# Kernel tuning notes

Measured on AMD Instinct MI355X. Metric: run time of the kernel, lower is better.

## Reference

```python
import jax, jax.numpy as jnp
import numpy as np

B, C, N, T = 32, 32, 512, 168
EMB = 40
K_NEI = 20
ALPHA = 3.0          # saturation rate in graph learning
GCN_DEPTH = 2
PROP_ALPHA = 0.05    # retaining ratio in mix-hop propagation
KERNELS = (2, 3, 6, 7)
DIL = 2
T_OUT = T - (max(KERNELS) - 1) * DIL   # 156
C_BR = C // len(KERNELS)               # 8 channels per inception branch
EPS = 1e-5


def _conv2d(x, w, b, dil):
    # x: (B,Cin,N,T), w: (Cout,Cin,1,k), temporal dilation dil
    y = jax.lax.conv_general_dilated(
        x, w, window_strides=(1, 1), padding='VALID',
        rhs_dilation=(1, dil), dimension_numbers=('NCHW', 'OIHW', 'NCHW'))
    return y + b[None, :, None, None]


def _inception(x, ws, bs):
    outs = [_conv2d(x, w, b, DIL) for w, b in zip(ws, bs)]
    tmin = outs[-1].shape[-1]   # largest kernel -> shortest output
    return jnp.concatenate([o[..., -tmin:] for o in outs], axis=1)


def setup_inputs() -> dict:
    key = jax.random.key(0)
    ks = jax.random.split(key, 32)
    d = {}
    d['x'] = jax.random.normal(ks[0], (B, C, N, T), jnp.float32)
    d['idx'] = jnp.arange(N)  # permutation of nodes (identity)
    # graph learning params
    d['emb1'] = jax.random.normal(ks[1], (N, EMB), jnp.float32)
    d['emb2'] = jax.random.normal(ks[2], (N, EMB), jnp.float32)
    d['W1'] = jax.random.normal(ks[3], (EMB, EMB), jnp.float32) * 0.15
    d['b1'] = jnp.zeros((EMB,), jnp.float32)
    d['W2'] = jax.random.normal(ks[4], (EMB, EMB), jnp.float32) * 0.15
    d['b2'] = jnp.zeros((EMB,), jnp.float32)
    # dilated inception filter/gate conv params
    i = 5
    for pre in ('f', 'g'):
        for k in KERNELS:
            d[f'{pre}w{k}'] = jax.random.normal(ks[i], (C_BR, C, 1, k), jnp.float32) * 0.05
            d[f'{pre}b{k}'] = jnp.zeros((C_BR,), jnp.float32)
            i += 1
    # mix-hop 1x1 mlp: (gcn_depth+1)*C -> C
    d['mlp_w'] = jax.random.normal(ks[i], (C, (GCN_DEPTH + 1) * C, 1, 1), jnp.float32) * 0.05
    d['mlp_b'] = jnp.zeros((C,), jnp.float32)
    # node-indexed layer norm affine params, shape (C, N, T_OUT)
    d['ln_w'] = jnp.ones((C, N, T_OUT), jnp.float32)
    d['ln_b'] = jnp.zeros((C, N, T_OUT), jnp.float32)
    return d


def reference(x, idx, emb1, emb2, W1, b1, W2, b2,
              fw2, fb2, fw3, fb3, fw6, fb6, fw7, fb7,
              gw2, gb2, gw3, gb3, gw6, gb6, gw7, gb7,
              mlp_w, mlp_b, ln_w, ln_b):
    # ---- graph learning: topk-masked adjacency (N,N) ----
    n1 = jnp.tanh(ALPHA * (emb1[idx] @ W1.T + b1))
    n2 = jnp.tanh(ALPHA * (emb2[idx] @ W2.T + b2))
    a = n1 @ n2.T - n2 @ n1.T
    A = jax.nn.relu(jnp.tanh(ALPHA * a))
    _, top_idx = jax.lax.top_k(A, K_NEI)                 # deterministic topk (torch adds rand*0.01 tiebreak)
    mask = jnp.zeros_like(A).at[jnp.arange(A.shape[0])[:, None], top_idx].set(1.0)
    A = A * mask

    # ---- dilated inception gated temporal conv ----
    filt = jnp.tanh(_inception(x, (fw2, fw3, fw6, fw7), (fb2, fb3, fb6, fb7)))
    gate = jax.nn.sigmoid(_inception(x, (gw2, gw3, gw6, gw7), (gb2, gb3, gb6, gb7)))
    z = filt * gate                                       # (B, C, N, T_OUT)

    # ---- mix-hop graph convolution ----
    Ah = A + jnp.eye(A.shape[0], dtype=A.dtype)
    Ah = Ah / Ah.sum(1, keepdims=True)                    # row-degree normalization
    h = z
    hops = [z]
    for _ in range(GCN_DEPTH):
        h = PROP_ALPHA * z + (1.0 - PROP_ALPHA) * jnp.einsum('bcwt,vw->bcvt', h, Ah)
        hops.append(h)
    h0 = jnp.concatenate(hops, axis=1)                    # (B, 3C, N, T_OUT)
    out = _conv2d(h0, mlp_w, mlp_b, 1)                    # 1x1 mlp -> (B, C, N, T_OUT)

    # ---- residual + node-indexed layer norm over dims (C,N,T) ----
    out = out + x[..., -T_OUT:]
    mean = out.mean(axis=(1, 2, 3), keepdims=True)
    var = out.var(axis=(1, 2, 3), keepdims=True)
    out = (out - mean) * jax.lax.rsqrt(var + EPS)
    out = out * ln_w[:, idx, :][None] + ln_b[:, idx, :][None]
    return out
```

## Files before the change

### kernel.cpp

```cpp
#include <hip/hip_runtime.h>

#define NB 32
#define NC 32
#define NNODE 512
#define NT 168
#define NTO 156
#define NQ 39
#define NEMB 40
#define KNEI 20
#define NADJ 21
#define ZT_PITCH 42
#define XROWS 176
#define NPB 4
#define CT (NC * NTO)
#define NPAIR (CT / 8)

static_assert(NTO == 4 * NQ, "t quads");

typedef __attribute__((ext_vector_type(8))) short bf16x8;
typedef __attribute__((ext_vector_type(16))) float f32x16;
typedef __attribute__((ext_vector_type(4))) float f32x4;
typedef __attribute__((ext_vector_type(8))) unsigned short u16x8;

__device__ __forceinline__ float fast_tanh(float x) {
  float e = __expf(2.0f * x);
  return 1.0f - 2.0f / (e + 1.0f);
}
__device__ __forceinline__ float fast_sigmoid(float x) {
  return 1.0f / (1.0f + __expf(-x));
}
__device__ __forceinline__ unsigned short f2b(float v) {
  unsigned int u = __float_as_uint(v);
  unsigned int r = (u + 0x7FFFu + ((u >> 16) & 1u)) >> 16;
  return (unsigned short)r;
}
__device__ __forceinline__ float b2f(unsigned short u) {
  return __uint_as_float((unsigned int)u << 16);
}
template <typename T>
__device__ __forceinline__ void pin(T& v) {
  f32x4 t = __builtin_bit_cast(f32x4, v);
  asm volatile("" : "+v"(t));
  v = __builtin_bit_cast(T, t);
}

__global__ __launch_bounds__(128) void g1_kernel(
    const float* __restrict__ emb1, const float* __restrict__ emb2,
    const float* __restrict__ W1, const float* __restrict__ b1,
    const float* __restrict__ W2, const float* __restrict__ b2,
    const int* __restrict__ idx, float* __restrict__ n1, float* __restrict__ n2) {
  const int v = blockIdx.x;
  const int tid = threadIdx.x;
  const int iv = idx[v];
  if (tid < NEMB) {
    float s = b1[tid];
    const float* er = emb1 + iv * NEMB;
    const float* wr = W1 + tid * NEMB;
    for (int f = 0; f < NEMB; ++f) s = fmaf(er[f], wr[f], s);
    n1[v * NEMB + tid] = tanhf(3.0f * s);
  } else if (tid >= 64 && tid < 64 + NEMB) {
    const int e = tid - 64;
    float s = b2[e];
    const float* er = emb2 + iv * NEMB;
    const float* wr = W2 + e * NEMB;
    for (int f = 0; f < NEMB; ++f) s = fmaf(er[f], wr[f], s);
    n2[v * NEMB + e] = tanhf(3.0f * s);
  }
}

__global__ __launch_bounds__(256) void g2_kernel(
    const float* __restrict__ n1, const float* __restrict__ n2,
    int* __restrict__ cols, float* __restrict__ wts) {
  const int v = blockIdx.x;
  const int tid = threadIdx.x;
  volatile __shared__ float Arow[NNODE];
  __shared__ float n1v[NEMB], n2v[NEMB];
  if (tid < NEMB) n1v[tid] = n1[v * NEMB + tid];
  if (tid >= 64 && tid < 64 + NEMB) n2v[tid - 64] = n2[v * NEMB + tid - 64];
  __syncthreads();
  for (int w = tid; w < NNODE; w += 256) {
    float d1 = 0.f, d2 = 0.f;
    const float* r1 = n1 + w * NEMB;
    const float* r2 = n2 + w * NEMB;
    for (int e = 0; e < NEMB; ++e) {
      d1 = fmaf(n1v[e], r2[e], d1);
      d2 = fmaf(n2v[e], r1[e], d2);
    }
    float a = tanhf(3.0f * (d1 - d2));
    Arow[w] = a > 0.f ? a : 0.f;
  }
  __syncthreads();
  if (tid >= 64) return;
  float sum = 1.0f;
  float selv[KNEI];
  int seli[KNEI];
  #pragma unroll
  for (int s = 0; s < KNEI; ++s) {
    float bv = -1.f; int bi = NNODE;
    #pragma unroll
    for (int w8 = 0; w8 < NNODE / 64; ++w8) {
      const int w = tid + 64 * w8;
      const float val = Arow[w];
      if (val > bv || (val == bv && w < bi)) { bv = val; bi = w; }
    }
    #pragma unroll
    for (int off = 32; off >= 1; off >>= 1) {
      const float ov = __shfl_down(bv, off);
      const int oi = __shfl_down(bi, off);
      if (ov > bv || (ov == bv && oi < bi)) { bv = ov; bi = oi; }
    }
    bv = __shfl(bv, 0);
    bi = __shfl(bi, 0);
    selv[s] = bv;
    seli[s] = bi;
    Arow[bi] = -2.f;
    sum += bv;
  }
  if (tid == 0) {
    const float inv = 1.0f / sum;
    #pragma unroll
    for (int s = 0; s < KNEI; ++s) {
      cols[v * NADJ + s] = seli[s];
      wts[v * NADJ + s] = selv[s] * inv;
    }
    cols[v * NADJ + KNEI] = v;
    wts[v * NADJ + KNEI] = inv;
  }
}

struct ZParams {
  const float* fw[4]; const float* fb[4];
  const float* gw[4]; const float* gb[4];
};

#define PA_CNT (2 * 2 * 7 * 64 * 8)
#define PB_CNT (2 * 64 * 16)
#define PNA_CNT (3 * 2 * 64 * 8)
__global__ __launch_bounds__(256) void pack_kernel(ZParams p, const float* __restrict__ mw,
                                                   unsigned short* __restrict__ pA,
                                                   float* __restrict__ pB,
                                                   unsigned short* __restrict__ pNA) {
  const int idx = blockIdx.x * 256 + threadIdx.x;
  if (idx < PA_CNT) {
    const int e = idx & 7;
    const int l = (idx >> 3) & 63;
    int rest = idx >> 9;
    const int j = rest % 7;
    rest /= 7;
    const int s = rest & 1;
    const int m = rest >> 1;
    const int row = l & 31;
    const int k = ((l >> 5) << 3) + e;
    const int ci = s * 16 + k;
    const int isF = (row < 16);
    const int co = m * 16 + (isF ? row : row - 16);
    const int br = co >> 3;
    const int kk = (br == 0) ? 2 : (br == 1) ? 3 : (br == 2) ? 6 : 7;
    const int jw = j - (7 - kk);
    const float* arr = isF ? p.fw[br] : p.gw[br];
    float val = (jw >= 0) ? arr[((co & 7) * NC + ci) * kk + jw] : 0.f;
    pA[idx] = f2b(val);
  } else if (idx < PA_CNT + PB_CNT) {
    const int ib = idx - PA_CNT;
    const int r = ib & 15;
    const int l = (ib >> 4) & 63;
    const int m = ib >> 10;
    const int rr = r & 7;
    const int row = (rr & 3) + 8 * (rr >> 2) + 4 * (l >> 5);
    const int co = m * 16 + row;
    const int br = co >> 3;
    const float* arr = (r < 8) ? p.fb[br] : p.gb[br];
    pB[ib] = arr[co & 7];
  } else if (idx < PA_CNT + PB_CNT + PNA_CNT) {
    const int in_ = idx - (PA_CNT + PB_CNT);
    const int e = in_ & 7;
    const int l = (in_ >> 3) & 63;
    const int s = (in_ >> 9) & 1;
    const int which = in_ >> 10;
    const int co = l & 31;
    const int c = s * 16 + ((l >> 5) << 3) + e;
    const float w0 = mw[co * 96 + c];
    const float w1 = mw[co * 96 + 32 + c];
    const float w2 = mw[co * 96 + 64 + c];
    float val;
    if (which == 0)      val = w0 + 0.05f * (w1 + w2);
    else if (which == 1) val = 0.95f * w1 + 0.0475f * w2;
    else                 val = 0.9025f * w2;
    pNA[in_] = f2b(val);
  }
}

__global__ __launch_bounds__(256) void xprep_kernel(
    const float* __restrict__ x, unsigned short* __restrict__ xbf) {
  const int n = blockIdx.x;
  const int b = blockIdx.y;
  const int tid = threadIdx.x;
  const int cp = tid & 15;
  const int t0 = tid >> 4;
  const float* xc0 = x + ((size_t)(b * NC + 2 * cp) * NNODE + n) * NT;
  const float* xc1 = xc0 + (size_t)NNODE * NT;
  unsigned int* dst = (unsigned int*)(xbf + (size_t)(b * NNODE + n) * (XROWS * NC));
  #pragma unroll
  for (int k = 0; k < 11; ++k) {
    const int t = t0 + 16 * k;
    unsigned int v = 0;
    if (t < NT) {
      v = (unsigned int)f2b(xc0[t]) | ((unsigned int)f2b(xc1[t]) << 16);
    }
    dst[t * 16 + cp] = v;
  }
}

__attribute__((amdgpu_waves_per_eu(2, 4)))
__global__ __launch_bounds__(256) void zs_kernel(
    const unsigned short* __restrict__ xbf, const unsigned short* __restrict__ pA,
    const float* __restrict__ pBias, const unsigned short* __restrict__ pNA,
    unsigned short* __restrict__ S) {
  __shared__ unsigned short zt[160 * ZT_PITCH];
  __shared__ unsigned short ot[96 * 160];
  const int n0 = blockIdx.x * NPB;
  const int b = blockIdx.y;
  const int tid = threadIdx.x;
  if (tid < 4 * ZT_PITCH) zt[156 * ZT_PITCH + tid] = 0;
  const int w = tid >> 6, l = tid & 63;
  const int jc = l & 31, h = l >> 5;
  const int m = w & 1;

  bf16x8 aF[2][7];
  #pragma unroll
  for (int s = 0; s < 2; ++s)
    #pragma unroll
    for (int j = 0; j < 7; ++j) {
      aF[s][j] = *reinterpret_cast<const bf16x8*>(
          pA + ((((m * 2 + s) * 7 + j) << 6) + l) * 8);
      pin(aF[s][j]);
    }
  f32x4 bias4[4];
  {
    const f32x4* pb4 = reinterpret_cast<const f32x4*>(pBias + (m * 64 + l) * 16);
    #pragma unroll
    for (int q = 0; q < 4; ++q) { bias4[q] = pb4[q]; pin(bias4[q]); }
  }
  bf16x8 nA[3][2];
  #pragma unroll
  for (int which = 0; which < 3; ++which)
    #pragma unroll
    for (int s = 0; s < 2; ++s) {
      nA[which][s] = *reinterpret_cast<const bf16x8*>(
          pNA + (((which * 2 + s) << 6) + l) * 8);
      pin(nA[which][s]);
    }

  for (int nn = 0; nn < NPB; ++nn) {
    const int n = n0 + nn;
    const unsigned short* xbn = xbf + (size_t)(b * NNODE + n) * (XROWS * NC);
    for (int tile = (w >> 1); tile < 5; tile += 2) {
      const int t0 = tile * 32;
      f32x16 acc;
      #pragma unroll
      for (int r = 0; r < 16; ++r) acc[r] = bias4[r >> 2][r & 3];
      const unsigned short* bp = xbn + (t0 + jc) * NC + h * 8;
      #pragma unroll
      for (int j = 0; j < 7; ++j) {
        bf16x8 b0 = *reinterpret_cast<const bf16x8*>(bp + 2 * j * NC);
        bf16x8 b1 = *reinterpret_cast<const bf16x8*>(bp + 2 * j * NC + 16);
        acc = __builtin_amdgcn_mfma_f32_32x32x16_bf16(aF[0][j], b0, acc, 0, 0, 0);
        acc = __builtin_amdgcn_mfma_f32_32x32x16_bf16(aF[1][j], b1, acc, 0, 0, 0);
      }
      const int t = t0 + jc;
      if (t < NTO) {
        #pragma unroll
        for (int r = 0; r < 8; ++r) {
          const float f = fast_tanh(acc[r]);
          const float g = fast_sigmoid(acc[r + 8]);
          const int row = (r & 3) + 8 * (r >> 2) + 4 * h;
          const int co = m * 16 + row;
          zt[t * ZT_PITCH + co] = f2b(f * g);
        }
      }
    }
    __syncthreads();
    #pragma unroll
    for (int mat = 0; mat < 3; ++mat) {
      #pragma unroll
      for (int tile = 0; tile < 5; ++tile) {
        if (((mat * 5 + tile) & 3) != w) continue;
        const int t0 = tile * 32;
        const unsigned short* zp = zt + (t0 + jc) * ZT_PITCH + h * 8;
        bf16x8 b0 = *reinterpret_cast<const bf16x8*>(zp);
        bf16x8 b1 = *reinterpret_cast<const bf16x8*>(zp + 16);
        f32x16 d;
        #pragma unroll
        for (int r = 0; r < 16; ++r) d[r] = 0.f;
        d = __builtin_amdgcn_mfma_f32_32x32x16_bf16(nA[mat][0], b0, d, 0, 0, 0);
        d = __builtin_amdgcn_mfma_f32_32x32x16_bf16(nA[mat][1], b1, d, 0, 0, 0);
        #pragma unroll
        for (int r = 0; r < 16; ++r) {
          const int row = (r & 3) + 8 * (r >> 2) + 4 * h;
          ot[(mat * 32 + row) * 160 + t0 + jc] = f2b(d[r]);
        }
      }
    }
    __syncthreads();
    unsigned short* Sbv = S + (size_t)(b * NNODE + n) * 3 * CT;
    for (int i = tid; i < 96 * NQ; i += 256) {
      const int row = i / NQ;
      const int qq = i - row * NQ;
      ushort4 v4 = *reinterpret_cast<const ushort4*>(ot + row * 160 + 4 * qq);
      *reinterpret_cast<ushort4*>(Sbv + 4 * i) = v4;
    }
  }
}

__global__ __launch_bounds__(256) void m_kernel(
    const unsigned short* __restrict__ S, const int* __restrict__ cols,
    const float* __restrict__ wts, unsigned short* __restrict__ M) {
  const int bid = blockIdx.x;
  const int v = bid & (NNODE - 1);
  const int b = bid >> 9;
  const int tid = threadIdx.x;
  float acc[3][8];
  const unsigned short* s1p = S + ((size_t)bid * 3 + 1) * CT;
  #pragma unroll
  for (int k = 0; k < 2; ++k) {
    u16x8 u = *reinterpret_cast<const u16x8*>(s1p + 8 * (tid + 256 * k));
    #pragma unroll
    for (int j = 0; j < 8; ++j) acc[k][j] = b2f(u[j]);
  }
  if (tid < NPAIR - 512) {
    u16x8 u = *reinterpret_cast<const u16x8*>(s1p + 8 * (tid + 512));
    #pragma unroll
    for (int j = 0; j < 8; ++j) acc[2][j] = b2f(u[j]);
  }
  for (int s = 0; s < NADJ; ++s) {
    const int col = cols[v * NADJ + s];
    const float w = wts[v * NADJ + s];
    const unsigned short* p = S + (((size_t)(b << 9) + col) * 3 + 2) * CT;
    #pragma unroll
    for (int k = 0; k < 2; ++k) {
      u16x8 u = *reinterpret_cast<const u16x8*>(p + 8 * (tid + 256 * k));
      #pragma unroll
      for (int j = 0; j < 8; ++j) acc[k][j] = fmaf(w, b2f(u[j]), acc[k][j]);
    }
    if (tid < NPAIR - 512) {
      u16x8 u = *reinterpret_cast<const u16x8*>(p + 8 * (tid + 512));
      #pragma unroll
      for (int j = 0; j < 8; ++j) acc[2][j] = fmaf(w, b2f(u[j]), acc[2][j]);
    }
  }
  unsigned short* mp = M + (size_t)bid * CT;
  #pragma unroll
  for (int k = 0; k < 2; ++k) {
    u16x8 o;
    #pragma unroll
    for (int j = 0; j < 8; ++j) o[j] = f2b(acc[k][j]);
    *reinterpret_cast<u16x8*>(mp + 8 * (tid + 256 * k)) = o;
  }
  if (tid < NPAIR - 512) {
    u16x8 o;
    #pragma unroll
    for (int j = 0; j < 8; ++j) o[j] = f2b(acc[2][j]);
    *reinterpret_cast<u16x8*>(mp + 8 * (tid + 512)) = o;
  }
}

__global__ __launch_bounds__(256) void f_kernel(
    const unsigned short* __restrict__ S, const unsigned short* __restrict__ M,
    const float* __restrict__ x, const int* __restrict__ cols,
    const float* __restrict__ wts, const float* __restrict__ mb,
    float* __restrict__ out, float* __restrict__ stats) {
  const int bid = blockIdx.x;
  const int v = bid & (NNODE - 1);
  const int b = bid >> 9;
  const int tid = threadIdx.x;
  __shared__ float mbs[NC];
  if (tid < NC) mbs[tid] = mb[tid];
  float acc[3][8];
  const unsigned short* s0p = S + (size_t)bid * 3 * CT;
  #pragma unroll
  for (int k = 0; k < 2; ++k) {
    u16x8 u = *reinterpret_cast<const u16x8*>(s0p + 8 * (tid + 256 * k));
    #pragma unroll
    for (int j = 0; j < 8; ++j) acc[k][j] = b2f(u[j]);
  }
  if (tid < NPAIR - 512) {
    u16x8 u = *reinterpret_cast<const u16x8*>(s0p + 8 * (tid + 512));
    #pragma unroll
    for (int j = 0; j < 8; ++j) acc[2][j] = b2f(u[j]);
  }
  for (int s = 0; s < NADJ; ++s) {
    const int col = cols[v * NADJ + s];
    const float w = wts[v * NADJ + s];
    const unsigned short* p = M + ((size_t)(b << 9) + col) * CT;
    #pragma unroll
    for (int k = 0; k < 2; ++k) {
      u16x8 u = *reinterpret_cast<const u16x8*>(p + 8 * (tid + 256 * k));
      #pragma unroll
      for (int j = 0; j < 8; ++j) acc[k][j] = fmaf(w, b2f(u[j]), acc[k][j]);
    }
    if (tid < NPAIR - 512) {
      u16x8 u = *reinterpret_cast<const u16x8*>(p + 8 * (tid + 512));
      #pragma unroll
      for (int j = 0; j < 8; ++j) acc[2][j] = fmaf(w, b2f(u[j]), acc[2][j]);
    }
  }
  __syncthreads();
  float st1 = 0.f, st2 = 0.f;
  #pragma unroll
  for (int k = 0; k < 3; ++k) {
    const int pi = tid + 256 * k;
    if (pi < NPAIR) {
      #pragma unroll
      for (int hh = 0; hh < 2; ++hh) {
        const int e = 8 * pi + 4 * hh;
        const int c = e / NTO;
        const int t = e - c * NTO;
        const float bias = mbs[c];
        const size_t rowb = ((size_t)(b * NC + c) * NNODE + v);
        const float4 xr = *reinterpret_cast<const float4*>(x + rowb * NT + 12 + t);
        float4 o;
        o.x = acc[k][4 * hh + 0] + bias + xr.x;
        o.y = acc[k][4 * hh + 1] + bias + xr.y;
        o.z = acc[k][4 * hh + 2] + bias + xr.z;
        o.w = acc[k][4 * hh + 3] + bias + xr.w;
        *reinterpret_cast<float4*>(out + rowb * NTO + t) = o;
        st1 += o.x + o.y + o.z + o.w;
        st2 += o.x * o.x + o.y * o.y + o.z * o.z + o.w * o.w;
      }
    }
  }
  #pragma unroll
  for (int off = 32; off >= 1; off >>= 1) {
    st1 += __shfl_down(st1, off);
    st2 += __shfl_down(st2, off);
  }
  __shared__ float r1[4], r2[4];
  const int lane = threadIdx.x & 63, wv_ = threadIdx.x >> 6;
  if (lane == 0) { r1[wv_] = st1; r2[wv_] = st2; }
  __syncthreads();
  if (threadIdx.x == 0) {
    atomicAdd(&stats[b * 2], r1[0] + r1[1] + r1[2] + r1[3]);
    atomicAdd(&stats[b * 2 + 1], r2[0] + r2[1] + r2[2] + r2[3]);
  }
}

__global__ __launch_bounds__(256) void ln_kernel(
    float* __restrict__ out, const float* __restrict__ lnw,
    const float* __restrict__ lnb, const int* __restrict__ idx,
    const float* __restrict__ stats) {
  const int i = blockIdx.x * 256 + threadIdx.x;
  const int q = i % NQ;
  const int r = i / NQ;
  const int v = r % NNODE;
  const int r2 = r / NNODE;
  const int co = r2 % NC;
  const int b = r2 / NC;
  const float invM = 1.0f / (float)(NC * NNODE * NTO);
  const float mean = stats[b * 2] * invM;
  const float var = stats[b * 2 + 1] * invM - mean * mean;
  const float rs = rsqrtf(var + 1e-5f);
  float4 o = *reinterpret_cast<const float4*>(out + 4 * i);
  const int iv = idx[v];
  const int lb = (co * NNODE + iv) * NTO + 4 * q;
  const float4 w = *reinterpret_cast<const float4*>(lnw + lb);
  const float4 bb = *reinterpret_cast<const float4*>(lnb + lb);
  o.x = (o.x - mean) * rs * w.x + bb.x;
  o.y = (o.y - mean) * rs * w.y + bb.y;
  o.z = (o.z - mean) * rs * w.z + bb.z;
  o.w = (o.w - mean) * rs * w.w + bb.w;
  *reinterpret_cast<float4*>(out + 4 * i) = o;
}

extern "C" void kernel_launch(void* const* d_in, const int* in_sizes, int n_in,
                              void* d_out, int out_size, void* d_ws, size_t ws_size,
                              hipStream_t stream) {
  const float* x    = (const float*)d_in[0];
  const int*   idx  = (const int*)d_in[1];
  const float* emb1 = (const float*)d_in[2];
  const float* emb2 = (const float*)d_in[3];
  const float* W1   = (const float*)d_in[4];
  const float* b1   = (const float*)d_in[5];
  const float* W2   = (const float*)d_in[6];
  const float* b2   = (const float*)d_in[7];
  const float* mlp_w = (const float*)d_in[24];
  const float* mlp_b = (const float*)d_in[25];
  const float* ln_w = (const float*)d_in[26];
  const float* ln_b = (const float*)d_in[27];

  char* ws = (char*)d_ws;
  float* n1    = (float*)(ws);
  float* n2    = (float*)(ws + (128 << 10));
  int*   cols  = (int*)  (ws + (256 << 10));
  float* wts   = (float*)(ws + (320 << 10));
  float* stats = (float*)(ws + (384 << 10));
  unsigned short* pA = (unsigned short*)(ws + (400 << 10));
  float* pBias = (float*)(ws + (440 << 10));
  unsigned short* pNA = (unsigned short*)(ws + (456 << 10));
  unsigned short* xbf = (unsigned short*)(ws + (512 << 10));
  const size_t xbf_elems = (size_t)NB * NNODE * XROWS * NC;
  unsigned short* S = xbf + xbf_elems;
  const size_t s_elems = (size_t)NB * NNODE * 3 * CT;
  unsigned short* M = S + s_elems;

  ZParams zp;
  for (int k = 0; k < 4; ++k) {
    zp.fw[k] = (const float*)d_in[8 + 2 * k];
    zp.fb[k] = (const float*)d_in[9 + 2 * k];
    zp.gw[k] = (const float*)d_in[16 + 2 * k];
    zp.gb[k] = (const float*)d_in[17 + 2 * k];
  }

  hipMemsetAsync(stats, 0, 2 * NB * sizeof(float), stream);
  g1_kernel<<<NNODE, 128, 0, stream>>>(emb1, emb2, W1, b1, W2, b2, idx, n1, n2);
  g2_kernel<<<NNODE, 256, 0, stream>>>(n1, n2, cols, wts);
  pack_kernel<<<76, 256, 0, stream>>>(zp, mlp_w, pA, pBias, pNA);
  xprep_kernel<<<dim3(NNODE, NB), 256, 0, stream>>>(x, xbf);
  zs_kernel<<<dim3(NNODE / NPB, NB), 256, 0, stream>>>(xbf, pA, pBias, pNA, S);
  m_kernel<<<NB * NNODE, 256, 0, stream>>>(S, cols, wts, M);
  f_kernel<<<NB * NNODE, 256, 0, stream>>>(S, M, x, cols, wts, mlp_b,
                                           (float*)d_out, stats);
  ln_kernel<<<NB * NC * NNODE * NQ / 256, 256, 0, stream>>>((float*)d_out, ln_w, ln_b,
                                                            idx, stats);
}
```

Before: 1.447 ms.

## Stage neighbor slabs in LDS for sparse graph propagation kernels

```diff
diff --git a/kernel.cpp b/kernel.cpp
--- a/kernel.cpp
+++ b/kernel.cpp
@@ -13,9 +13,12 @@
 #define XROWS 176
 #define NPB 4
 #define CT (NC * NTO)
-#define NPAIR (CT / 8)
+#define GW 32
+#define GP 34
+#define NCHUNK (CT / GW)
 
 static_assert(NTO == 4 * NQ, "t quads");
+static_assert(CT == GW * NCHUNK, "chunks");
 
 typedef __attribute__((ext_vector_type(8))) short bf16x8;
 typedef __attribute__((ext_vector_type(16))) float f32x16;
@@ -312,117 +315,111 @@
   }
 }
 
-__global__ __launch_bounds__(256) void m_kernel(
+__global__ __launch_bounds__(256) void m2_kernel(
     const unsigned short* __restrict__ S, const int* __restrict__ cols,
     const float* __restrict__ wts, unsigned short* __restrict__ M) {
-  const int bid = blockIdx.x;
-  const int v = bid & (NNODE - 1);
-  const int b = bid >> 9;
+  const int c0 = blockIdx.x * GW;
+  const int b = blockIdx.y;
   const int tid = threadIdx.x;
-  float acc[3][8];
-  const unsigned short* s1p = S + ((size_t)bid * 3 + 1) * CT;
-  #pragma unroll
-  for (int k = 0; k < 2; ++k) {
-    u16x8 u = *reinterpret_cast<const u16x8*>(s1p + 8 * (tid + 256 * k));
-    #pragma unroll
-    for (int j = 0; j < 8; ++j) acc[k][j] = b2f(u[j]);
-  }
-  if (tid < NPAIR - 512) {
-    u16x8 u = *reinterpret_cast<const u16x8*>(s1p + 8 * (tid + 512));
-    #pragma unroll
-    for (int j = 0; j < 8; ++j) acc[2][j] = b2f(u[j]);
-  }
-  for (int s = 0; s < NADJ; ++s) {
-    const int col = cols[v * NADJ + s];
-    const float w = wts[v * NADJ + s];
-    const unsigned short* p = S + (((size_t)(b << 9) + col) * 3 + 2) * CT;
-    #pragma unroll
-    for (int k = 0; k < 2; ++k) {
-      u16x8 u = *reinterpret_cast<const u16x8*>(p + 8 * (tid + 256 * k));
-      #pragma unroll
-      for (int j = 0; j < 8; ++j) acc[k][j] = fmaf(w, b2f(u[j]), acc[k][j]);
-    }
-    if (tid < NPAIR - 512) {
-      u16x8 u = *reinterpret_cast<const u16x8*>(p + 8 * (tid + 512));
-      #pragma unroll
-      for (int j = 0; j < 8; ++j) acc[2][j] = fmaf(w, b2f(u[j]), acc[2][j]);
-    }
-  }
-  unsigned short* mp = M + (size_t)bid * CT;
-  #pragma unroll
-  for (int k = 0; k < 2; ++k) {
-    u16x8 o;
-    #pragma unroll
-    for (int j = 0; j < 8; ++j) o[j] = f2b(acc[k][j]);
-    *reinterpret_cast<u16x8*>(mp + 8 * (tid + 256 * k)) = o;
-  }
-  if (tid < NPAIR - 512) {
-    u16x8 o;
-    #pragma unroll
-    for (int j = 0; j < 8; ++j) o[j] = f2b(acc[2][j]);
-    *reinterpret_cast<u16x8*>(mp + 8 * (tid + 512)) = o;
-  }
-}
-
-__global__ __launch_bounds__(256) void f_kernel(
+  __shared__ unsigned short slab[NNODE * GP];
+  for (int i = tid; i < NNODE * (GW / 8); i += 256) {
+    const int v = i >> 2, g = i & 3;
+    u16x8 u = *reinterpret_cast<const u16x8*>(
+        S + (((size_t)(b << 9) + v) * 3 + 2) * CT + c0 + 8 * g);
+    *reinterpret_cast<u16x8*>(slab + v * GP + 8 * g) = u;
+  }
+  __syncthreads();
+  #pragma unroll
+  for (int it = 0; it < NNODE / 256; ++it) {
+    const int v = tid + 256 * it;
+    const size_t base = (size_t)(b << 9) + v;
+    float acc[4][8];
+    #pragma unroll
+    for (int g = 0; g < 4; ++g) {
+      u16x8 u = *reinterpret_cast<const u16x8*>(S + (base * 3 + 1) * CT + c0 + 8 * g);
+      #pragma unroll
+      for (int j = 0; j < 8; ++j) acc[g][j] = b2f(u[j]);
+    }
+    const int* cv = cols + v * NADJ;
+    const float* wv = wts + v * NADJ;
+    for (int s = 0; s < NADJ; ++s) {
+      const int col = cv[s];
+      const float w = wv[s];
+      const unsigned short* rp = slab + col * GP;
+      #pragma unroll
+      for (int g = 0; g < 4; ++g) {
+        u16x8 u = *reinterpret_cast<const u16x8*>(rp + 8 * g);
+        #pragma unroll
+        for (int j = 0; j < 8; ++j) acc[g][j] = fmaf(w, b2f(u[j]), acc[g][j]);
+      }
+    }
+    unsigned short* mp = M + base * CT + c0;
+    #pragma unroll
+    for (int g = 0; g < 4; ++g) {
+      u16x8 o;
+      #pragma unroll
+      for (int j = 0; j < 8; ++j) o[j] = f2b(acc[g][j]);
+      *reinterpret_cast<u16x8*>(mp + 8 * g) = o;
+    }
+  }
+}
+
+__global__ __launch_bounds__(256) void f2_kernel(
     const unsigned short* __restrict__ S, const unsigned short* __restrict__ M,
     const float* __restrict__ x, const int* __restrict__ cols,
     const float* __restrict__ wts, const float* __restrict__ mb,
     float* __restrict__ out, float* __restrict__ stats) {
-  const int bid = blockIdx.x;
-  const int v = bid & (NNODE - 1);
-  const int b = bid >> 9;
+  const int c0 = blockIdx.x * GW;
+  const int b = blockIdx.y;
   const int tid = threadIdx.x;
-  __shared__ float mbs[NC];
-  if (tid < NC) mbs[tid] = mb[tid];
-  float acc[3][8];
-  const unsigned short* s0p = S + (size_t)bid * 3 * CT;
-  #pragma unroll
-  for (int k = 0; k < 2; ++k) {
-    u16x8 u = *reinterpret_cast<const u16x8*>(s0p + 8 * (tid + 256 * k));
-    #pragma unroll
-    for (int j = 0; j < 8; ++j) acc[k][j] = b2f(u[j]);
-  }
-  if (tid < NPAIR - 512) {
-    u16x8 u = *reinterpret_cast<const u16x8*>(s0p + 8 * (tid + 512));
-    #pragma unroll
-    for (int j = 0; j < 8; ++j) acc[2][j] = b2f(u[j]);
-  }
-  for (int s = 0; s < NADJ; ++s) {
-    const int col = cols[v * NADJ + s];
-    const float w = wts[v * NADJ + s];
-    const unsigned short* p = M + ((size_t)(b << 9) + col) * CT;
-    #pragma unroll
-    for (int k = 0; k < 2; ++k) {
-      u16x8 u = *reinterpret_cast<const u16x8*>(p + 8 * (tid + 256 * k));
-      #pragma unroll
-      for (int j = 0; j < 8; ++j) acc[k][j] = fmaf(w, b2f(u[j]), acc[k][j]);
-    }
-    if (tid < NPAIR - 512) {
-      u16x8 u = *reinterpret_cast<const u16x8*>(p + 8 * (tid + 512));
-      #pragma unroll
-      for (int j = 0; j < 8; ++j) acc[2][j] = fmaf(w, b2f(u[j]), acc[2][j]);
-    }
+  __shared__ unsigned short slab[NNODE * GP];
+  for (int i = tid; i < NNODE * (GW / 8); i += 256) {
+    const int v = i >> 2, g = i & 3;
+    u16x8 u = *reinterpret_cast<const u16x8*>(
+        M + ((size_t)(b << 9) + v) * CT + c0 + 8 * g);
+    *reinterpret_cast<u16x8*>(slab + v * GP + 8 * g) = u;
   }
   __syncthreads();
   float st1 = 0.f, st2 = 0.f;
   #pragma unroll
-  for (int k = 0; k < 3; ++k) {
-    const int pi = tid + 256 * k;
-    if (pi < NPAIR) {
-      #pragma unroll
-      for (int hh = 0; hh < 2; ++hh) {
-        const int e = 8 * pi + 4 * hh;
+  for (int it = 0; it < NNODE / 256; ++it) {
+    const int v = tid + 256 * it;
+    const size_t base = (size_t)(b << 9) + v;
+    float acc[4][8];
+    #pragma unroll
+    for (int g = 0; g < 4; ++g) {
+      u16x8 u = *reinterpret_cast<const u16x8*>(S + base * 3 * CT + c0 + 8 * g);
+      #pragma unroll
+      for (int j = 0; j < 8; ++j) acc[g][j] = b2f(u[j]);
+    }
+    const int* cv = cols + v * NADJ;
+    const float* wv = wts + v * NADJ;
+    for (int s = 0; s < NADJ; ++s) {
+      const int col = cv[s];
+      const float w = wv[s];
+      const unsigned short* rp = slab + col * GP;
+      #pragma unroll
+      for (int g = 0; g < 4; ++g) {
+        u16x8 u = *reinterpret_cast<const u16x8*>(rp + 8 * g);
+        #pragma unroll
+        for (int j = 0; j < 8; ++j) acc[g][j] = fmaf(w, b2f(u[j]), acc[g][j]);
+      }
+    }
+    #pragma unroll
+    for (int g = 0; g < 4; ++g) {
+      #pragma unroll
+      for (int q = 0; q < 2; ++q) {
+        const int e = c0 + 8 * g + 4 * q;
         const int c = e / NTO;
         const int t = e - c * NTO;
-        const float bias = mbs[c];
         const size_t rowb = ((size_t)(b * NC + c) * NNODE + v);
+        const float bias = mb[c];
         const float4 xr = *reinterpret_cast<const float4*>(x + rowb * NT + 12 + t);
         float4 o;
-        o.x = acc[k][4 * hh + 0] + bias + xr.x;
-        o.y = acc[k][4 * hh + 1] + bias + xr.y;
-        o.z = acc[k][4 * hh + 2] + bias + xr.z;
-        o.w = acc[k][4 * hh + 3] + bias + xr.w;
+        o.x = acc[g][4 * q + 0] + bias + xr.x;
+        o.y = acc[g][4 * q + 1] + bias + xr.y;
+        o.z = acc[g][4 * q + 2] + bias + xr.z;
+        o.w = acc[g][4 * q + 3] + bias + xr.w;
         *reinterpret_cast<float4*>(out + rowb * NTO + t) = o;
         st1 += o.x + o.y + o.z + o.w;
         st2 += o.x * o.x + o.y * o.y + o.z * o.z + o.w * o.w;
@@ -435,10 +432,10 @@
     st2 += __shfl_down(st2, off);
   }
   __shared__ float r1[4], r2[4];
-  const int lane = threadIdx.x & 63, wv_ = threadIdx.x >> 6;
+  const int lane = tid & 63, wv_ = tid >> 6;
   if (lane == 0) { r1[wv_] = st1; r2[wv_] = st2; }
   __syncthreads();
-  if (threadIdx.x == 0) {
+  if (tid == 0) {
     atomicAdd(&stats[b * 2], r1[0] + r1[1] + r1[2] + r1[3]);
     atomicAdd(&stats[b * 2 + 1], r2[0] + r2[1] + r2[2] + r2[3]);
   }
@@ -516,9 +513,9 @@
   pack_kernel<<<76, 256, 0, stream>>>(zp, mlp_w, pA, pBias, pNA);
   xprep_kernel<<<dim3(NNODE, NB), 256, 0, stream>>>(x, xbf);
   zs_kernel<<<dim3(NNODE / NPB, NB), 256, 0, stream>>>(xbf, pA, pBias, pNA, S);
-  m_kernel<<<NB * NNODE, 256, 0, stream>>>(S, cols, wts, M);
-  f_kernel<<<NB * NNODE, 256, 0, stream>>>(S, M, x, cols, wts, mlp_b,
-                                           (float*)d_out, stats);
+  m2_kernel<<<dim3(NCHUNK, NB), 256, 0, stream>>>(S, cols, wts, M);
+  f2_kernel<<<dim3(NCHUNK, NB), 256, 0, stream>>>(S, M, x, cols, wts, mlp_b,
+                                                  (float*)d_out, stats);
   ln_kernel<<<NB * NC * NNODE * NQ / 256, 256, 0, stream>>>((float*)d_out, ln_w, ln_b,
                                                             idx, stats);
 }
```

After: 1.842 ms. 1.27x slower.

## Write zs outputs directly to global and stage pre-norm output in bf16

Applied to the files above, without the earlier changes.

```diff
diff --git a/kernel.cpp b/kernel.cpp
--- a/kernel.cpp
+++ b/kernel.cpp
@@ -217,7 +217,6 @@
     const float* __restrict__ pBias, const unsigned short* __restrict__ pNA,
     unsigned short* __restrict__ S) {
   __shared__ unsigned short zt[160 * ZT_PITCH];
-  __shared__ unsigned short ot[96 * 160];
   const int n0 = blockIdx.x * NPB;
   const int b = blockIdx.y;
   const int tid = threadIdx.x;
@@ -280,6 +279,7 @@
       }
     }
     __syncthreads();
+    unsigned short* Sbv = S + (size_t)(b * NNODE + n) * 3 * CT;
     #pragma unroll
     for (int mat = 0; mat < 3; ++mat) {
       #pragma unroll
@@ -294,21 +294,18 @@
         for (int r = 0; r < 16; ++r) d[r] = 0.f;
         d = __builtin_amdgcn_mfma_f32_32x32x16_bf16(nA[mat][0], b0, d, 0, 0, 0);
         d = __builtin_amdgcn_mfma_f32_32x32x16_bf16(nA[mat][1], b1, d, 0, 0, 0);
-        #pragma unroll
-        for (int r = 0; r < 16; ++r) {
-          const int row = (r & 3) + 8 * (r >> 2) + 4 * h;
-          ot[(mat * 32 + row) * 160 + t0 + jc] = f2b(d[r]);
+        const int t = t0 + jc;
+        if (t < NTO) {
+          unsigned short* so = Sbv + (size_t)mat * CT + (size_t)(4 * h) * NTO + t;
+          #pragma unroll
+          for (int r = 0; r < 16; ++r) {
+            const int row = (r & 3) + 8 * (r >> 2);
+            so[row * NTO] = f2b(d[r]);
+          }
         }
       }
     }
     __syncthreads();
-    unsigned short* Sbv = S + (size_t)(b * NNODE + n) * 3 * CT;
-    for (int i = tid; i < 96 * NQ; i += 256) {
-      const int row = i / NQ;
-      const int qq = i - row * NQ;
-      ushort4 v4 = *reinterpret_cast<const ushort4*>(ot + row * 160 + 4 * qq);
-      *reinterpret_cast<ushort4*>(Sbv + 4 * i) = v4;
-    }
   }
 }
 
@@ -368,7 +365,7 @@
     const unsigned short* __restrict__ S, const unsigned short* __restrict__ M,
     const float* __restrict__ x, const int* __restrict__ cols,
     const float* __restrict__ wts, const float* __restrict__ mb,
-    float* __restrict__ out, float* __restrict__ stats) {
+    unsigned short* __restrict__ P, float* __restrict__ stats) {
   const int bid = blockIdx.x;
   const int v = bid & (NNODE - 1);
   const int b = bid >> 9;
@@ -423,7 +420,9 @@
         o.y = acc[k][4 * hh + 1] + bias + xr.y;
         o.z = acc[k][4 * hh + 2] + bias + xr.z;
         o.w = acc[k][4 * hh + 3] + bias + xr.w;
-        *reinterpret_cast<float4*>(out + rowb * NTO + t) = o;
+        ushort4 o4;
+        o4.x = f2b(o.x); o4.y = f2b(o.y); o4.z = f2b(o.z); o4.w = f2b(o.w);
+        *reinterpret_cast<ushort4*>(P + rowb * NTO + t) = o4;
         st1 += o.x + o.y + o.z + o.w;
         st2 += o.x * o.x + o.y * o.y + o.z * o.z + o.w * o.w;
       }
@@ -445,9 +444,9 @@
 }
 
 __global__ __launch_bounds__(256) void ln_kernel(
-    float* __restrict__ out, const float* __restrict__ lnw,
-    const float* __restrict__ lnb, const int* __restrict__ idx,
-    const float* __restrict__ stats) {
+    const unsigned short* __restrict__ P, float* __restrict__ out,
+    const float* __restrict__ lnw, const float* __restrict__ lnb,
+    const int* __restrict__ idx, const float* __restrict__ stats) {
   const int i = blockIdx.x * 256 + threadIdx.x;
   const int q = i % NQ;
   const int r = i / NQ;
@@ -459,15 +458,16 @@
   const float mean = stats[b * 2] * invM;
   const float var = stats[b * 2 + 1] * invM - mean * mean;
   const float rs = rsqrtf(var + 1e-5f);
-  float4 o = *reinterpret_cast<const float4*>(out + 4 * i);
+  ushort4 u = *reinterpret_cast<const ushort4*>(P + 4 * i);
   const int iv = idx[v];
   const int lb = (co * NNODE + iv) * NTO + 4 * q;
   const float4 w = *reinterpret_cast<const float4*>(lnw + lb);
   const float4 bb = *reinterpret_cast<const float4*>(lnb + lb);
-  o.x = (o.x - mean) * rs * w.x + bb.x;
-  o.y = (o.y - mean) * rs * w.y + bb.y;
-  o.z = (o.z - mean) * rs * w.z + bb.z;
-  o.w = (o.w - mean) * rs * w.w + bb.w;
+  float4 o;
+  o.x = (b2f(u.x) - mean) * rs * w.x + bb.x;
+  o.y = (b2f(u.y) - mean) * rs * w.y + bb.y;
+  o.z = (b2f(u.z) - mean) * rs * w.z + bb.z;
+  o.w = (b2f(u.w) - mean) * rs * w.w + bb.w;
   *reinterpret_cast<float4*>(out + 4 * i) = o;
 }
 
@@ -501,6 +501,7 @@
   unsigned short* S = xbf + xbf_elems;
   const size_t s_elems = (size_t)NB * NNODE * 3 * CT;
   unsigned short* M = S + s_elems;
+  unsigned short* P = xbf;
 
   ZParams zp;
   for (int k = 0; k < 4; ++k) {
@@ -517,8 +518,7 @@
   xprep_kernel<<<dim3(NNODE, NB), 256, 0, stream>>>(x, xbf);
   zs_kernel<<<dim3(NNODE / NPB, NB), 256, 0, stream>>>(xbf, pA, pBias, pNA, S);
   m_kernel<<<NB * NNODE, 256, 0, stream>>>(S, cols, wts, M);
-  f_kernel<<<NB * NNODE, 256, 0, stream>>>(S, M, x, cols, wts, mlp_b,
-                                           (float*)d_out, stats);
-  ln_kernel<<<NB * NC * NNODE * NQ / 256, 256, 0, stream>>>((float*)d_out, ln_w, ln_b,
-                                                            idx, stats);
-}
+  f_kernel<<<NB * NNODE, 256, 0, stream>>>(S, M, x, cols, wts, mlp_b, P, stats);
+  ln_kernel<<<NB * NC * NNODE * NQ / 256, 256, 0, stream>>>(P, (float*)d_out, ln_w,
+                                                            ln_b, idx, stats);
+}
```

Result: faster. 1.389 ms (-4.0%).
